# Optimization experiments

Measured on AMD Instinct MI355X. Metric: run time of the kernel, lower is better.

Reference implementation:

```python
import jax, jax.numpy as jnp
import numpy as np

D_MODEL = 768
D_STATE = 16
D_CONV = 4
D_INNER = 2 * D_MODEL          # expand=2
DT_RANK = (D_MODEL + 15) // 16 # ceil(d_model/16), official Mamba default
N_LAYERS = 4
N_VOCAB = 2048
LN_EPS = 1e-5


def _silu(x):
    return x * jax.nn.sigmoid(x)


def _layer_norm(x, g, b):
    mu = jnp.mean(x, axis=-1, keepdims=True)
    var = jnp.mean(jnp.square(x - mu), axis=-1, keepdims=True)
    return (x - mu) * jax.lax.rsqrt(var + LN_EPS) * g + b


def _mamba_block(x, W_in, conv_w, conv_b, W_x, W_dt, b_dt, A_log, D_skip, W_out):
    # x: [B, L, D_MODEL]
    Bsz, L, _ = x.shape
    xz = x @ W_in                              # [B, L, 2*D_INNER]
    xc, z = jnp.split(xz, 2, axis=-1)
    # causal depthwise conv over time
    xt = xc.transpose(0, 2, 1)                 # [B, D_INNER, L]
    kern = conv_w[:, None, :]                  # [D_INNER, 1, D_CONV]
    xt = jax.lax.conv_general_dilated(
        xt, kern, window_strides=(1,), padding=[(D_CONV - 1, 0)],
        dimension_numbers=('NCH', 'OIH', 'NCH'), feature_group_count=D_INNER)
    u = _silu(xt.transpose(0, 2, 1) + conv_b)  # [B, L, D_INNER]
    # input-dependent SSM params
    dbl = u @ W_x                              # [B, L, DT_RANK + 2*D_STATE]
    dt, Bm, Cm = jnp.split(dbl, [DT_RANK, DT_RANK + D_STATE], axis=-1)
    delta = jax.nn.softplus(dt @ W_dt + b_dt)  # [B, L, D_INNER]
    A = -jnp.exp(A_log)                        # [D_INNER, D_STATE], negative

    def step(h, inp):
        d_t, B_t, C_t, u_t = inp               # [B,Di],[B,N],[B,N],[B,Di]
        dA = jnp.exp(d_t[..., None] * A)       # [B, D_INNER, D_STATE]
        dBu = (d_t * u_t)[..., None] * B_t[:, None, :]
        h = dA * h + dBu
        y = jnp.einsum('bdn,bn->bd', h, C_t)
        return h, y

    h0 = jnp.zeros((Bsz, D_INNER, D_STATE), x.dtype)
    _, ys = jax.lax.scan(step, h0, (delta.transpose(1, 0, 2),
                                    Bm.transpose(1, 0, 2),
                                    Cm.transpose(1, 0, 2),
                                    u.transpose(1, 0, 2)))
    y = ys.transpose(1, 0, 2) + u * D_skip     # skip connection D*u
    y = y * _silu(z)                           # gating
    return y @ W_out                           # [B, L, D_MODEL]


def setup_inputs() -> dict:
    key = jax.random.key(0)
    ks = jax.random.split(key, 12)
    B, L = 2, 2048
    s = 0.02
    tokens = jax.random.randint(ks[0], (B, L), 0, N_VOCAB)
    emb = jax.random.normal(ks[1], (N_VOCAB + 1, D_MODEL), jnp.float32) * s
    emb = emb.at[N_VOCAB].set(0.0)  # padding_idx row
    in_proj_w = jax.random.normal(ks[2], (N_LAYERS, D_MODEL, 2 * D_INNER), jnp.float32) * s
    conv_w = jax.random.normal(ks[3], (N_LAYERS, D_INNER, D_CONV), jnp.float32) * s
    conv_b = jnp.zeros((N_LAYERS, D_INNER), jnp.float32)
    x_proj_w = jax.random.normal(ks[4], (N_LAYERS, D_INNER, DT_RANK + 2 * D_STATE), jnp.float32) * s
    dt_proj_w = jax.random.normal(ks[5], (N_LAYERS, DT_RANK, D_INNER), jnp.float32) * s
    # dt bias so softplus(bias) lands in [1e-3, 0.1] (standard Mamba dt init)
    dt = jnp.exp(jax.random.uniform(ks[6], (N_LAYERS, D_INNER)) * (np.log(0.1) - np.log(1e-3)) + np.log(1e-3))
    dt_proj_b = dt + jnp.log(-jnp.expm1(-dt))  # inverse softplus
    A_log = jnp.log(jnp.tile(jnp.arange(1, D_STATE + 1, dtype=jnp.float32), (N_LAYERS, D_INNER, 1)))
    skip_D = jnp.ones((N_LAYERS, D_INNER), jnp.float32)
    out_proj_w = jax.random.normal(ks[7], (N_LAYERS, D_INNER, D_MODEL), jnp.float32) * s
    ln_g = jnp.ones((N_LAYERS, D_MODEL), jnp.float32)
    ln_b = jnp.zeros((N_LAYERS, D_MODEL), jnp.float32)
    head_w = jax.random.normal(ks[8], (D_MODEL, N_VOCAB), jnp.float32) * s
    head_b = jnp.zeros((N_VOCAB,), jnp.float32)
    return dict(tokens=tokens, emb=emb, in_proj_w=in_proj_w, conv_w=conv_w,
                conv_b=conv_b, x_proj_w=x_proj_w, dt_proj_w=dt_proj_w,
                dt_proj_b=dt_proj_b, A_log=A_log, skip_D=skip_D,
                out_proj_w=out_proj_w, ln_g=ln_g, ln_b=ln_b,
                head_w=head_w, head_b=head_b)


def reference(tokens, emb, in_proj_w, conv_w, conv_b, x_proj_w, dt_proj_w,
              dt_proj_b, A_log, skip_D, out_proj_w, ln_g, ln_b, head_w, head_b):
    x = emb[tokens]                            # [B, L, D_MODEL]
    for i in range(N_LAYERS):                  # post-norm residual (prenorm=False)
        z = _mamba_block(x, in_proj_w[i], conv_w[i], conv_b[i], x_proj_w[i],
                         dt_proj_w[i], dt_proj_b[i], A_log[i], skip_D[i],
                         out_proj_w[i])
        x = x + z                              # dropout=0 (identity)
        x = _layer_norm(x, ln_g[i], ln_b[i])
    return x @ head_w + head_b                 # [B, L, N_VOCAB]
```

## Files before the change

kernel.cpp:

```cpp
#include <hip/hip_runtime.h>
#include <hip/hip_bf16.h>
#include <math.h>

#define BSZ 2
#define SEQ 2048
#define DM 768
#define DI 1536
#define DS 16
#define DTR 48
#define NL 4
#define NV 2048
#define LNEPS 1e-5f
#define MROWS (BSZ * SEQ)
#define CCH 32
#define TCH 64
#define KSPLIT 12

typedef __hip_bfloat16 bf16;
typedef unsigned short u16t;
typedef __attribute__((ext_vector_type(8))) short short8;
typedef __attribute__((ext_vector_type(4))) float f32x4;

__device__ __forceinline__ bool probe_bf16(const void* p) {
    const u16t* q = (const u16t*)p;
    return q[0] == 0x3F80 && q[1] == 0x3F80;
}
__device__ __forceinline__ float ldany(const void* p, size_t i, bool bf) {
    if (bf) {
        unsigned u = (unsigned)(((const u16t*)p)[i]) << 16;
        return __uint_as_float(u);
    }
    return ((const float*)p)[i];
}
__device__ __forceinline__ float ldb(const bf16* p, size_t i) { return __bfloat162float(p[i]); }
__device__ __forceinline__ void stb(bf16* p, size_t i, float v) { p[i] = __float2bfloat16(v); }
__device__ __forceinline__ u16t f2bbits(float f) {
    unsigned x = __float_as_uint(f);
    return (u16t)((x + 0x7fffu + ((x >> 16) & 1u)) >> 16);
}
__device__ __forceinline__ u16t ld_bfbits(const void* p, size_t i, bool bf) {
    if (bf) return ((const u16t*)p)[i];
    return f2bbits(((const float*)p)[i]);
}
__device__ __forceinline__ float softplus_fast(float x) {
    if (x > 20.f) return x;
    return 0.69314718056f * __log2f(1.f + __expf(x));
}
__device__ __forceinline__ float siluf(float x) { return x / (1.f + __expf(-x)); }

__global__ __launch_bounds__(256) void embed_kernel(const int* __restrict__ tokens,
                                                    const void* __restrict__ emb,
                                                    bf16* __restrict__ X,
                                                    const void* __restrict__ probe) {
    bool bf = probe_bf16(probe);
    int idx = blockIdx.x * 256 + threadIdx.x;
    if (idx >= MROWS * DM) return;
    int c = idx % DM;
    int bl = idx / DM;
    stb(X, idx, ldany(emb, (size_t)tokens[bl] * DM + c, bf));
}

__global__ __launch_bounds__(256) void transpose_w(const void* __restrict__ W, size_t woff,
                                                   bf16* __restrict__ WT, int K, int N,
                                                   const void* __restrict__ probe) {
    bool bf = probe_bf16(probe);
    __shared__ u16t T[64][65];
    const int n0 = blockIdx.x * 64, k0 = blockIdx.y * 64;
    const int tid = threadIdx.x;
#pragma unroll
    for (int it = 0; it < 16; ++it) {
        int j = tid + 256 * it;
        int r = j >> 6, c = j & 63;
        T[r][c] = ld_bfbits(W, woff + (size_t)(k0 + r) * N + n0 + c, bf);
    }
    __syncthreads();
#pragma unroll
    for (int it = 0; it < 2; ++it) {
        int j = tid + 256 * it;
        int c = j >> 3, r8 = (j & 7) * 8;
        u16t tmp[8];
#pragma unroll
        for (int e = 0; e < 8; ++e) tmp[e] = T[r8 + e][c];
        *reinterpret_cast<uint4*>(WT + (size_t)(n0 + c) * K + k0 + r8) =
            *reinterpret_cast<const uint4*>(tmp);
    }
}

template <int MODE>
__global__ __launch_bounds__(256) void gemm_bt(const bf16* __restrict__ A, int lda,
                                               const bf16* __restrict__ BT,
                                               const void* __restrict__ bias, size_t bioff,
                                               bf16* __restrict__ Cb, void* __restrict__ Cout,
                                               int N, int K,
                                               const void* __restrict__ probe) {
    __shared__ u16t Alds[128 * 40];
    __shared__ u16t Blds[128 * 40];
    const int tid = threadIdx.x;
    const int lane = tid & 63, w = tid >> 6;
    const int wr = w >> 1, wc = w & 1;
    const int l15 = lane & 15, l4 = lane >> 4;
    const int row0 = blockIdx.y * 128, col0 = blockIdx.x * 128;
    f32x4 acc[4][4];
#pragma unroll
    for (int i = 0; i < 4; ++i)
#pragma unroll
        for (int j = 0; j < 4; ++j) acc[i][j] = (f32x4){0.f, 0.f, 0.f, 0.f};

    for (int k0 = 0; k0 < K; k0 += 32) {
#pragma unroll
        for (int j = 0; j < 2; ++j) {
            int i = tid + 256 * j;
            int r = i >> 2, c8 = (i & 3) * 8;
            uint4 va = *reinterpret_cast<const uint4*>(A + (size_t)(row0 + r) * lda + k0 + c8);
            *reinterpret_cast<uint4*>(&Alds[r * 40 + c8]) = va;
            uint4 vb = *reinterpret_cast<const uint4*>(BT + (size_t)(col0 + r) * K + k0 + c8);
            *reinterpret_cast<uint4*>(&Blds[r * 40 + c8]) = vb;
        }
        __syncthreads();
        short8 af[4], bfr[4];
#pragma unroll
        for (int fi = 0; fi < 4; ++fi)
            af[fi] = *reinterpret_cast<const short8*>(&Alds[(wr * 64 + fi * 16 + l15) * 40 + l4 * 8]);
#pragma unroll
        for (int fj = 0; fj < 4; ++fj)
            bfr[fj] = *reinterpret_cast<const short8*>(&Blds[(wc * 64 + fj * 16 + l15) * 40 + l4 * 8]);
#pragma unroll
        for (int fi = 0; fi < 4; ++fi)
#pragma unroll
            for (int fj = 0; fj < 4; ++fj)
                acc[fi][fj] = __builtin_amdgcn_mfma_f32_16x16x32_bf16(af[fi], bfr[fj],
                                                                      acc[fi][fj], 0, 0, 0);
        __syncthreads();
    }
    bool bf = probe_bf16(probe);
#pragma unroll
    for (int fi = 0; fi < 4; ++fi) {
        int row = row0 + wr * 64 + fi * 16 + l4 * 4;
#pragma unroll
        for (int fj = 0; fj < 4; ++fj) {
            int col = col0 + wc * 64 + fj * 16 + l15;
#pragma unroll
            for (int r = 0; r < 4; ++r) {
                float v = acc[fi][fj][r];
                size_t off = (size_t)(row + r) * N + col;
                if (MODE == 2) {
                    float o = v + ldany(bias, bioff + col, bf);
                    if (bf) stb((bf16*)Cout, off, o);
                    else ((float*)Cout)[off] = o;
                } else {
                    stb(Cb, off, v);
                }
            }
        }
    }
}

__global__ __launch_bounds__(256) void xproj_mfma(const bf16* __restrict__ A,
                                                  const void* __restrict__ B, size_t boff,
                                                  float* __restrict__ XPART,
                                                  const void* __restrict__ probe) {
    bool bf = probe_bf16(probe);
    __shared__ u16t Alds[128 * 40];
    __shared__ u16t Blds[80 * 40];
    const int tid = threadIdx.x;
    const int lane = tid & 63, w = tid >> 6;
    const int l15 = lane & 15, l4 = lane >> 4;
    const int z = blockIdx.x, row0 = blockIdx.y * 128;
    f32x4 acc[2][5];
#pragma unroll
    for (int i = 0; i < 2; ++i)
#pragma unroll
        for (int j = 0; j < 5; ++j) acc[i][j] = (f32x4){0.f, 0.f, 0.f, 0.f};

    for (int ks = 0; ks < 4; ++ks) {
        int kbase = z * 128 + ks * 32;
#pragma unroll
        for (int j = 0; j < 2; ++j) {
            int i = tid + 256 * j;
            int r = i >> 2, c8 = (i & 3) * 8;
            uint4 v = *reinterpret_cast<const uint4*>(A + (size_t)(row0 + r) * DI + kbase + c8);
            *reinterpret_cast<uint4*>(&Alds[r * 40 + c8]) = v;
        }
        for (int i = tid; i < 320; i += 256) {
            int kk = i / 10, c8 = (i % 10) * 8;
            u16t tmp[8];
            if (bf) {
                uint4 v = *reinterpret_cast<const uint4*>((const u16t*)B + boff +
                                                          (size_t)(kbase + kk) * 80 + c8);
                const u16t* s = (const u16t*)&v;
#pragma unroll
                for (int e = 0; e < 8; ++e) tmp[e] = s[e];
            } else {
                const float* Bf = (const float*)B + boff + (size_t)(kbase + kk) * 80 + c8;
#pragma unroll
                for (int e = 0; e < 8; ++e) tmp[e] = f2bbits(Bf[e]);
            }
#pragma unroll
            for (int e = 0; e < 8; ++e) Blds[(c8 + e) * 40 + kk] = tmp[e];
        }
        __syncthreads();
        short8 af[2], bfr[5];
#pragma unroll
        for (int fi = 0; fi < 2; ++fi)
            af[fi] = *reinterpret_cast<const short8*>(&Alds[(w * 32 + fi * 16 + l15) * 40 + l4 * 8]);
#pragma unroll
        for (int fj = 0; fj < 5; ++fj)
            bfr[fj] = *reinterpret_cast<const short8*>(&Blds[(fj * 16 + l15) * 40 + l4 * 8]);
#pragma unroll
        for (int fi = 0; fi < 2; ++fi)
#pragma unroll
            for (int fj = 0; fj < 5; ++fj)
                acc[fi][fj] = __builtin_amdgcn_mfma_f32_16x16x32_bf16(af[fi], bfr[fj],
                                                                      acc[fi][fj], 0, 0, 0);
        __syncthreads();
    }
#pragma unroll
    for (int fi = 0; fi < 2; ++fi) {
        int row = row0 + w * 32 + fi * 16 + l4 * 4;
#pragma unroll
        for (int fj = 0; fj < 5; ++fj) {
            int col = fj * 16 + l15;
#pragma unroll
            for (int r = 0; r < 4; ++r)
                XPART[((size_t)z * MROWS + row + r) * 80 + col] = acc[fi][fj][r];
        }
    }
}

__global__ __launch_bounds__(256) void xreduce_kernel(const float* __restrict__ XPART,
                                                      bf16* __restrict__ DBL) {
    int idx = blockIdx.x * 256 + threadIdx.x;
    float s = 0.f;
#pragma unroll
    for (int z = 0; z < KSPLIT; ++z) s += XPART[(size_t)z * MROWS * 80 + idx];
    stb(DBL, idx, s);
}

__global__ __launch_bounds__(256) void dtproj_valu(const bf16* __restrict__ DBL,
                                                   const void* __restrict__ Wdt, size_t woff,
                                                   const void* __restrict__ bias, size_t bioff,
                                                   bf16* __restrict__ DELTA,
                                                   const void* __restrict__ probe) {
    bool bf = probe_bf16(probe);
    __shared__ float Wlds[48 * 132];
    __shared__ float Dlds[64 * 49];
    const int tid = threadIdx.x;
    const int tx = tid & 15, ty = tid >> 4;
    const int col0 = blockIdx.x * 128, rows0 = blockIdx.y * 64;
#pragma unroll
    for (int it = 0; it < 24; ++it) {
        int j = tid + 256 * it;
        int k = j >> 7, c = j & 127;
        Wlds[k * 132 + c] = ldany(Wdt, woff + (size_t)k * DI + col0 + c, bf);
    }
#pragma unroll
    for (int it = 0; it < 12; ++it) {
        int j = tid + 256 * it;
        int r = j / 48, k = j % 48;
        Dlds[r * 49 + k] = ldb(DBL, (size_t)(rows0 + r) * 80 + k);
    }
    __syncthreads();
    float acc[4][8] = {};
#pragma unroll 4
    for (int k = 0; k < 48; ++k) {
        float4 w0 = *reinterpret_cast<const float4*>(&Wlds[k * 132 + tx * 8]);
        float4 w1 = *reinterpret_cast<const float4*>(&Wlds[k * 132 + tx * 8 + 4]);
        float wv[8] = {w0.x, w0.y, w0.z, w0.w, w1.x, w1.y, w1.z, w1.w};
#pragma unroll
        for (int r = 0; r < 4; ++r) {
            float d = Dlds[(ty * 4 + r) * 49 + k];
#pragma unroll
            for (int e = 0; e < 8; ++e) acc[r][e] += d * wv[e];
        }
    }
    float bj[8];
#pragma unroll
    for (int e = 0; e < 8; ++e) bj[e] = ldany(bias, bioff + col0 + tx * 8 + e, bf);
#pragma unroll
    for (int r = 0; r < 4; ++r) {
        u16t tmp[8];
#pragma unroll
        for (int e = 0; e < 8; ++e) tmp[e] = f2bbits(softplus_fast(acc[r][e] + bj[e]));
        *reinterpret_cast<uint4*>(DELTA + (size_t)(rows0 + ty * 4 + r) * DI + col0 + tx * 8) =
            *reinterpret_cast<const uint4*>(tmp);
    }
}

__global__ __launch_bounds__(256) void conv_silu_kernel(const bf16* __restrict__ XZ,
                                                        const void* __restrict__ cw, size_t cwoff,
                                                        const void* __restrict__ cb, size_t cboff,
                                                        bf16* __restrict__ U,
                                                        const void* __restrict__ probe) {
    bool bf = probe_bf16(probe);
    int idx = blockIdx.x * 256 + threadIdx.x;
    if (idx >= MROWS * DI) return;
    int d = idx % DI;
    int bl = idx / DI;
    int l = bl % SEQ;
    int b = bl / SEQ;
    float s = ldany(cb, cboff + d, bf);
#pragma unroll
    for (int k = 0; k < 4; ++k) {
        int lt = l - 3 + k;
        if (lt >= 0)
            s += ldany(cw, cwoff + d * 4 + k, bf) * ldb(XZ, ((size_t)(b * SEQ + lt)) * (2 * DI) + d);
    }
    stb(U, idx, siluf(s));
}

__global__ __launch_bounds__(256) void scan_phase1(const bf16* __restrict__ DELTA,
                                                   const bf16* __restrict__ U,
                                                   const bf16* __restrict__ DBL,
                                                   const void* __restrict__ A_log, size_t aoff,
                                                   float* __restrict__ P, float* __restrict__ Q,
                                                   const void* __restrict__ probe) {
    bool bf = probe_bf16(probe);
    int blk = blockIdx.x;
    int dt = blk % (DI / 256);
    int t2 = blk / (DI / 256);
    int c = t2 % CCH;
    int b = t2 / CCH;
    int d = dt * 256 + threadIdx.x;
    float An[16], h[16], q[16];
#pragma unroll
    for (int n = 0; n < 16; ++n) {
        An[n] = -__expf(ldany(A_log, aoff + (size_t)d * DS + n, bf));
        h[n] = 0.f;
        q[n] = 1.f;
    }
    int t0 = c * TCH;
    const bf16* dp = DELTA + (size_t)(b * SEQ + t0) * DI + d;
    const bf16* up = U + (size_t)(b * SEQ + t0) * DI + d;
    const u16t* bcp = (const u16t*)DBL + (size_t)(b * SEQ + t0) * 80 + DTR;
    float del = ldb(dp, 0), u = ldb(up, 0);
    uint4 b0 = *reinterpret_cast<const uint4*>(bcp);
    uint4 b1 = *reinterpret_cast<const uint4*>(bcp + 8);
    for (int t = 0; t < TCH; ++t) {
        float delc = del, uc = u;
        uint4 c0 = b0, c1 = b1;
        if (t + 1 < TCH) {
            dp += DI; up += DI; bcp += 80;
            del = ldb(dp, 0);
            u = ldb(up, 0);
            b0 = *reinterpret_cast<const uint4*>(bcp);
            b1 = *reinterpret_cast<const uint4*>(bcp + 8);
        }
        float du = delc * uc;
        const u16t* bs0 = (const u16t*)&c0;
        const u16t* bs1 = (const u16t*)&c1;
#pragma unroll
        for (int n = 0; n < 16; ++n) {
            float Bn = __uint_as_float((unsigned)(n < 8 ? bs0[n] : bs1[n - 8]) << 16);
            float dA = __expf(delc * An[n]);
            h[n] = dA * h[n] + du * Bn;
            q[n] *= dA;
        }
    }
    size_t o = ((((size_t)b * CCH + c) * DI) + d) * 16;
#pragma unroll
    for (int n = 0; n < 16; ++n) {
        P[o + n] = h[n];
        Q[o + n] = q[n];
    }
}

__global__ __launch_bounds__(256) void scan_phase2(const float* __restrict__ P,
                                                   const float* __restrict__ Q,
                                                   float* __restrict__ H0) {
    int g = blockIdx.x * 256 + threadIdx.x;
    int n = g & 15;
    int rest = g >> 4;
    int d = rest % DI;
    int b = rest / DI;
    float S = 0.f;
    for (int c = 0; c < CCH; ++c) {
        size_t idx = ((((size_t)b * CCH + c) * DI) + d) * 16 + n;
        H0[idx] = S;
        S = Q[idx] * S + P[idx];
    }
}

__global__ __launch_bounds__(256) void scan_phase3(const bf16* __restrict__ DELTA,
                                                   bf16* __restrict__ U,
                                                   const bf16* __restrict__ DBL,
                                                   const bf16* __restrict__ XZ,
                                                   const float* __restrict__ H0,
                                                   const void* __restrict__ A_log, size_t aoff,
                                                   const void* __restrict__ Dskip, size_t doff,
                                                   const void* __restrict__ probe) {
    bool bf = probe_bf16(probe);
    int blk = blockIdx.x;
    int dt = blk % (DI / 256);
    int t2 = blk / (DI / 256);
    int c = t2 % CCH;
    int b = t2 / CCH;
    int d = dt * 256 + threadIdx.x;
    float An[16], h[16];
    size_t ho = ((((size_t)b * CCH + c) * DI) + d) * 16;
#pragma unroll
    for (int n = 0; n < 16; ++n) {
        An[n] = -__expf(ldany(A_log, aoff + (size_t)d * DS + n, bf));
        h[n] = H0[ho + n];
    }
    float Dk = ldany(Dskip, doff + d, bf);
    int t0 = c * TCH;
    const bf16* dp = DELTA + (size_t)(b * SEQ + t0) * DI + d;
    bf16* ub = U;
    const bf16* zp = XZ + (size_t)(b * SEQ + t0) * 2 * DI + DI + d;
    const u16t* bcp = (const u16t*)DBL + (size_t)(b * SEQ + t0) * 80 + DTR;
    const bf16* up = U + (size_t)(b * SEQ + t0) * DI + d;
    float del = ldb(dp, 0), u = ldb(up, 0), z = ldb(zp, 0);
    uint4 b0 = *reinterpret_cast<const uint4*>(bcp);
    uint4 b1 = *reinterpret_cast<const uint4*>(bcp + 8);
    uint4 b2 = *reinterpret_cast<const uint4*>(bcp + 16);
    uint4 b3 = *reinterpret_cast<const uint4*>(bcp + 24);
    for (int t = 0; t < TCH; ++t) {
        float delc = del, uc = u, zc = z;
        uint4 c0 = b0, c1 = b1, c2 = b2, c3 = b3;
        if (t + 1 < TCH) {
            dp += DI; up += DI; zp += 2 * DI; bcp += 80;
            del = ldb(dp, 0);
            u = ldb(up, 0);
            z = ldb(zp, 0);
            b0 = *reinterpret_cast<const uint4*>(bcp);
            b1 = *reinterpret_cast<const uint4*>(bcp + 8);
            b2 = *reinterpret_cast<const uint4*>(bcp + 16);
            b3 = *reinterpret_cast<const uint4*>(bcp + 24);
        }
        float du = delc * uc;
        const u16t* bs0 = (const u16t*)&c0;
        const u16t* bs1 = (const u16t*)&c1;
        const u16t* cs0 = (const u16t*)&c2;
        const u16t* cs1 = (const u16t*)&c3;
        float y = 0.f;
#pragma unroll
        for (int n = 0; n < 16; ++n) {
            float Bn = __uint_as_float((unsigned)(n < 8 ? bs0[n] : bs1[n - 8]) << 16);
            float Cn = __uint_as_float((unsigned)(n < 8 ? cs0[n] : cs1[n - 8]) << 16);
            float dA = __expf(delc * An[n]);
            h[n] = dA * h[n] + du * Bn;
            y += h[n] * Cn;
        }
        stb(ub, (size_t)(b * SEQ + t0 + t) * DI + d, (y + uc * Dk) * siluf(zc));
    }
}

__global__ __launch_bounds__(256) void add_ln_kernel(const bf16* __restrict__ O,
                                                     bf16* __restrict__ X,
                                                     const void* __restrict__ g, size_t goff,
                                                     const void* __restrict__ be, size_t beoff,
                                                     const void* __restrict__ probe) {
    bool bf = probe_bf16(probe);
    int row = blockIdx.x;
    __shared__ float buf[DM];
    __shared__ float wred[8];
    __shared__ float stat[2];
    float part = 0.f;
    for (int c = threadIdx.x; c < DM; c += 256) {
        float v = ldb(X, (size_t)row * DM + c) + ldb(O, (size_t)row * DM + c);
        buf[c] = v;
        part += v;
    }
    for (int o = 32; o > 0; o >>= 1) part += __shfl_down(part, o, 64);
    int wid = threadIdx.x >> 6, lane = threadIdx.x & 63;
    if (lane == 0) wred[wid] = part;
    __syncthreads();
    if (threadIdx.x == 0) {
        float s = 0.f;
        for (int i = 0; i < 4; ++i) s += wred[i];
        stat[0] = s / DM;
    }
    __syncthreads();
    float mean = stat[0];
    float p2 = 0.f;
    for (int c = threadIdx.x; c < DM; c += 256) {
        float dv = buf[c] - mean;
        p2 += dv * dv;
    }
    for (int o = 32; o > 0; o >>= 1) p2 += __shfl_down(p2, o, 64);
    if (lane == 0) wred[4 + wid] = p2;
    __syncthreads();
    if (threadIdx.x == 0) {
        float s = 0.f;
        for (int i = 0; i < 4; ++i) s += wred[4 + i];
        stat[1] = rsqrtf(s / DM + LNEPS);
    }
    __syncthreads();
    float rs = stat[1];
    for (int c = threadIdx.x; c < DM; c += 256) {
        stb(X, (size_t)row * DM + c,
            (buf[c] - mean) * rs * ldany(g, goff + c, bf) + ldany(be, beoff + c, bf));
    }
}

extern "C" void kernel_launch(void* const* d_in, const int* in_sizes, int n_in,
                              void* d_out, int out_size, void* d_ws, size_t ws_size,
                              hipStream_t stream) {
    const int* tokens = (const int*)d_in[0];
    const void* emb = d_in[1];
    const void* in_proj_w = d_in[2];
    const void* conv_w = d_in[3];
    const void* conv_b = d_in[4];
    const void* x_proj_w = d_in[5];
    const void* dt_proj_w = d_in[6];
    const void* dt_proj_b = d_in[7];
    const void* A_log = d_in[8];
    const void* skip_D = d_in[9];
    const void* out_proj_w = d_in[10];
    const void* ln_g = d_in[11];
    const void* ln_b = d_in[12];
    const void* head_w = d_in[13];
    const void* head_b = d_in[14];
    const void* probe = ln_g;

    bf16* X = (bf16*)d_ws;
    bf16* XZ = X + (size_t)MROWS * DM;
    bf16* Ub = XZ + (size_t)MROWS * 2 * DI;
    bf16* DBL = Ub + (size_t)MROWS * DI;
    bf16* DELTA = DBL + (size_t)MROWS * 80;
    bf16* O = DELTA;
    float* P = (float*)(DELTA + (size_t)MROWS * DI);
    float* Q = P + (size_t)BSZ * CCH * DI * 16;
    float* H0 = Q + (size_t)BSZ * CCH * DI * 16;
    float* XPART = P;
    bf16* WT1 = (bf16*)(H0 + (size_t)BSZ * CCH * DI * 16);
    bf16* WT2 = WT1 + (size_t)(2 * DI) * DM;

    embed_kernel<<<(MROWS * DM + 255) / 256, 256, 0, stream>>>(tokens, emb, X, probe);

    for (int i = 0; i < NL; ++i) {
        transpose_w<<<dim3(2 * DI / 64, DM / 64), 256, 0, stream>>>(
            in_proj_w, (size_t)i * DM * 2 * DI, WT1, DM, 2 * DI, probe);
        transpose_w<<<dim3(DM / 64, DI / 64), 256, 0, stream>>>(
            out_proj_w, (size_t)i * DI * DM, WT2, DI, DM, probe);
        gemm_bt<0><<<dim3(2 * DI / 128, MROWS / 128), 256, 0, stream>>>(
            X, DM, WT1, nullptr, 0, XZ, nullptr, 2 * DI, DM, probe);
        conv_silu_kernel<<<(MROWS * DI + 255) / 256, 256, 0, stream>>>(
            XZ, conv_w, (size_t)i * DI * 4, conv_b, (size_t)i * DI, Ub, probe);
        xproj_mfma<<<dim3(KSPLIT, MROWS / 128), 256, 0, stream>>>(
            Ub, x_proj_w, (size_t)i * DI * 80, XPART, probe);
        xreduce_kernel<<<(MROWS * 80) / 256, 256, 0, stream>>>(XPART, DBL);
        dtproj_valu<<<dim3(DI / 128, MROWS / 64), 256, 0, stream>>>(
            DBL, dt_proj_w, (size_t)i * DTR * DI, dt_proj_b, (size_t)i * DI, DELTA, probe);
        scan_phase1<<<BSZ * CCH * (DI / 256), 256, 0, stream>>>(
            DELTA, Ub, DBL, A_log, (size_t)i * DI * DS, P, Q, probe);
        scan_phase2<<<(BSZ * DI * 16) / 256, 256, 0, stream>>>(P, Q, H0);
        scan_phase3<<<BSZ * CCH * (DI / 256), 256, 0, stream>>>(
            DELTA, Ub, DBL, XZ, H0, A_log, (size_t)i * DI * DS, skip_D, (size_t)i * DI, probe);
        gemm_bt<0><<<dim3(DM / 128, MROWS / 128), 256, 0, stream>>>(
            Ub, DI, WT2, nullptr, 0, O, nullptr, DM, DI, probe);
        add_ln_kernel<<<MROWS, 256, 0, stream>>>(O, X, ln_g, (size_t)i * DM, ln_b,
                                                 (size_t)i * DM, probe);
    }
    transpose_w<<<dim3(NV / 64, DM / 64), 256, 0, stream>>>(head_w, 0, WT1, DM, NV, probe);
    gemm_bt<2><<<dim3(NV / 128, MROWS / 128), 256, 0, stream>>>(
        X, DM, WT1, head_b, 0, nullptr, d_out, NV, DM, probe);
}
```

Before: 1.245 ms.

## Split scan state across thread pairs and vectorize conv and layernorm kernels

The scan phases 1 and 3 now assign two threads per channel, each owning 8 of the 16 state entries, which doubles the thread count to raise parallelism and cuts per-thread registers. Phase 3 combines the two partial outputs with a lane shuffle. The conv+SiLU kernel processes 8 channels per thread with 128-bit loads and stores, and add+LayerNorm uses 192 threads holding 4 values each in registers instead of a shared buffer. The pair split duplicates the delta/u/z loads per thread pair in exchange for more occupancy.

New measurement: 1.352 ms. 8.6% more time.

```diff
diff --git a/kernel.cpp b/kernel.cpp
--- a/kernel.cpp
+++ b/kernel.cpp
@@ -34,6 +34,7 @@
 }
 __device__ __forceinline__ float ldb(const bf16* p, size_t i) { return __bfloat162float(p[i]); }
 __device__ __forceinline__ void stb(bf16* p, size_t i, float v) { p[i] = __float2bfloat16(v); }
+__device__ __forceinline__ float bits2f(u16t b) { return __uint_as_float((unsigned)b << 16); }
 __device__ __forceinline__ u16t f2bbits(float f) {
     unsigned x = __float_as_uint(f);
     return (u16t)((x + 0x7fffu + ((x >> 16) & 1u)) >> 16);
@@ -286,26 +287,37 @@
     }
 }
 
-__global__ __launch_bounds__(256) void conv_silu_kernel(const bf16* __restrict__ XZ,
-                                                        const void* __restrict__ cw, size_t cwoff,
-                                                        const void* __restrict__ cb, size_t cboff,
-                                                        bf16* __restrict__ U,
-                                                        const void* __restrict__ probe) {
+__global__ __launch_bounds__(256) void conv_silu_v8(const bf16* __restrict__ XZ,
+                                                    const void* __restrict__ cw, size_t cwoff,
+                                                    const void* __restrict__ cb, size_t cboff,
+                                                    bf16* __restrict__ U,
+                                                    const void* __restrict__ probe) {
     bool bf = probe_bf16(probe);
     int idx = blockIdx.x * 256 + threadIdx.x;
-    if (idx >= MROWS * DI) return;
-    int d = idx % DI;
-    int bl = idx / DI;
+    int dp = idx % (DI / 8);
+    int bl = idx / (DI / 8);
+    int d0 = dp * 8;
     int l = bl % SEQ;
     int b = bl / SEQ;
-    float s = ldany(cb, cboff + d, bf);
+    float s[8];
+#pragma unroll
+    for (int e = 0; e < 8; ++e) s[e] = ldany(cb, cboff + d0 + e, bf);
 #pragma unroll
     for (int k = 0; k < 4; ++k) {
         int lt = l - 3 + k;
-        if (lt >= 0)
-            s += ldany(cw, cwoff + d * 4 + k, bf) * ldb(XZ, ((size_t)(b * SEQ + lt)) * (2 * DI) + d);
-    }
-    stb(U, idx, siluf(s));
+        if (lt < 0) continue;
+        uint4 v = *reinterpret_cast<const uint4*>((const u16t*)XZ +
+                                                  (size_t)(b * SEQ + lt) * 2 * DI + d0);
+        const u16t* xv = (const u16t*)&v;
+#pragma unroll
+        for (int e = 0; e < 8; ++e)
+            s[e] += ldany(cw, cwoff + (size_t)(d0 + e) * 4 + k, bf) * bits2f(xv[e]);
+    }
+    u16t out[8];
+#pragma unroll
+    for (int e = 0; e < 8; ++e) out[e] = f2bbits(siluf(s[e]));
+    *reinterpret_cast<uint4*>((u16t*)U + (size_t)bl * DI + d0) =
+        *reinterpret_cast<const uint4*>(out);
 }
 
 __global__ __launch_bounds__(256) void scan_phase1(const bf16* __restrict__ DELTA,
@@ -316,52 +328,49 @@
                                                    const void* __restrict__ probe) {
     bool bf = probe_bf16(probe);
     int blk = blockIdx.x;
-    int dt = blk % (DI / 256);
-    int t2 = blk / (DI / 256);
+    int dt = blk % (2 * DI / 256);
+    int t2 = blk / (2 * DI / 256);
     int c = t2 % CCH;
     int b = t2 / CCH;
-    int d = dt * 256 + threadIdx.x;
-    float An[16], h[16], q[16];
-#pragma unroll
-    for (int n = 0; n < 16; ++n) {
-        An[n] = -__expf(ldany(A_log, aoff + (size_t)d * DS + n, bf));
+    int g = dt * 256 + threadIdx.x;
+    int d = g >> 1, s = g & 1;
+    float An[8], h[8], q[8];
+#pragma unroll
+    for (int n = 0; n < 8; ++n) {
+        An[n] = -__expf(ldany(A_log, aoff + (size_t)d * DS + s * 8 + n, bf));
         h[n] = 0.f;
         q[n] = 1.f;
     }
     int t0 = c * TCH;
-    const bf16* dp = DELTA + (size_t)(b * SEQ + t0) * DI + d;
+    const bf16* dpp = DELTA + (size_t)(b * SEQ + t0) * DI + d;
     const bf16* up = U + (size_t)(b * SEQ + t0) * DI + d;
-    const u16t* bcp = (const u16t*)DBL + (size_t)(b * SEQ + t0) * 80 + DTR;
-    float del = ldb(dp, 0), u = ldb(up, 0);
+    const u16t* bcp = (const u16t*)DBL + (size_t)(b * SEQ + t0) * 80 + DTR + s * 8;
+    float del = ldb(dpp, 0), u = ldb(up, 0);
     uint4 b0 = *reinterpret_cast<const uint4*>(bcp);
-    uint4 b1 = *reinterpret_cast<const uint4*>(bcp + 8);
     for (int t = 0; t < TCH; ++t) {
         float delc = del, uc = u;
-        uint4 c0 = b0, c1 = b1;
+        uint4 c0 = b0;
         if (t + 1 < TCH) {
-            dp += DI; up += DI; bcp += 80;
-            del = ldb(dp, 0);
+            dpp += DI; up += DI; bcp += 80;
+            del = ldb(dpp, 0);
             u = ldb(up, 0);
             b0 = *reinterpret_cast<const uint4*>(bcp);
-            b1 = *reinterpret_cast<const uint4*>(bcp + 8);
         }
         float du = delc * uc;
-        const u16t* bs0 = (const u16t*)&c0;
-        const u16t* bs1 = (const u16t*)&c1;
-#pragma unroll
-        for (int n = 0; n < 16; ++n) {
-            float Bn = __uint_as_float((unsigned)(n < 8 ? bs0[n] : bs1[n - 8]) << 16);
+        const u16t* bs = (const u16t*)&c0;
+#pragma unroll
+        for (int n = 0; n < 8; ++n) {
+            float Bn = bits2f(bs[n]);
             float dA = __expf(delc * An[n]);
             h[n] = dA * h[n] + du * Bn;
             q[n] *= dA;
         }
     }
-    size_t o = ((((size_t)b * CCH + c) * DI) + d) * 16;
-#pragma unroll
-    for (int n = 0; n < 16; ++n) {
-        P[o + n] = h[n];
-        Q[o + n] = q[n];
-    }
+    size_t o = ((((size_t)b * CCH + c) * DI) + d) * 16 + s * 8;
+    *reinterpret_cast<float4*>(&P[o]) = (float4){h[0], h[1], h[2], h[3]};
+    *reinterpret_cast<float4*>(&P[o + 4]) = (float4){h[4], h[5], h[6], h[7]};
+    *reinterpret_cast<float4*>(&Q[o]) = (float4){q[0], q[1], q[2], q[3]};
+    *reinterpret_cast<float4*>(&Q[o + 4]) = (float4){q[4], q[5], q[6], q[7]};
 }
 
 __global__ __launch_bounds__(256) void scan_phase2(const float* __restrict__ P,
@@ -390,107 +399,102 @@
                                                    const void* __restrict__ probe) {
     bool bf = probe_bf16(probe);
     int blk = blockIdx.x;
-    int dt = blk % (DI / 256);
-    int t2 = blk / (DI / 256);
+    int dt = blk % (2 * DI / 256);
+    int t2 = blk / (2 * DI / 256);
     int c = t2 % CCH;
     int b = t2 / CCH;
-    int d = dt * 256 + threadIdx.x;
-    float An[16], h[16];
-    size_t ho = ((((size_t)b * CCH + c) * DI) + d) * 16;
-#pragma unroll
-    for (int n = 0; n < 16; ++n) {
-        An[n] = -__expf(ldany(A_log, aoff + (size_t)d * DS + n, bf));
+    int g = dt * 256 + threadIdx.x;
+    int d = g >> 1, s = g & 1;
+    float An[8], h[8];
+    size_t ho = ((((size_t)b * CCH + c) * DI) + d) * 16 + s * 8;
+#pragma unroll
+    for (int n = 0; n < 8; ++n) {
+        An[n] = -__expf(ldany(A_log, aoff + (size_t)d * DS + s * 8 + n, bf));
         h[n] = H0[ho + n];
     }
     float Dk = ldany(Dskip, doff + d, bf);
     int t0 = c * TCH;
-    const bf16* dp = DELTA + (size_t)(b * SEQ + t0) * DI + d;
-    bf16* ub = U;
+    const bf16* dpp = DELTA + (size_t)(b * SEQ + t0) * DI + d;
     const bf16* zp = XZ + (size_t)(b * SEQ + t0) * 2 * DI + DI + d;
-    const u16t* bcp = (const u16t*)DBL + (size_t)(b * SEQ + t0) * 80 + DTR;
+    const u16t* bcp = (const u16t*)DBL + (size_t)(b * SEQ + t0) * 80 + DTR + s * 8;
     const bf16* up = U + (size_t)(b * SEQ + t0) * DI + d;
-    float del = ldb(dp, 0), u = ldb(up, 0), z = ldb(zp, 0);
+    float del = ldb(dpp, 0), u = ldb(up, 0), z = ldb(zp, 0);
     uint4 b0 = *reinterpret_cast<const uint4*>(bcp);
-    uint4 b1 = *reinterpret_cast<const uint4*>(bcp + 8);
-    uint4 b2 = *reinterpret_cast<const uint4*>(bcp + 16);
-    uint4 b3 = *reinterpret_cast<const uint4*>(bcp + 24);
+    uint4 b1 = *reinterpret_cast<const uint4*>(bcp + 16);
     for (int t = 0; t < TCH; ++t) {
         float delc = del, uc = u, zc = z;
-        uint4 c0 = b0, c1 = b1, c2 = b2, c3 = b3;
+        uint4 c0 = b0, c1 = b1;
         if (t + 1 < TCH) {
-            dp += DI; up += DI; zp += 2 * DI; bcp += 80;
-            del = ldb(dp, 0);
+            dpp += DI; up += DI; zp += 2 * DI; bcp += 80;
+            del = ldb(dpp, 0);
             u = ldb(up, 0);
             z = ldb(zp, 0);
             b0 = *reinterpret_cast<const uint4*>(bcp);
-            b1 = *reinterpret_cast<const uint4*>(bcp + 8);
-            b2 = *reinterpret_cast<const uint4*>(bcp + 16);
-            b3 = *reinterpret_cast<const uint4*>(bcp + 24);
+            b1 = *reinterpret_cast<const uint4*>(bcp + 16);
         }
         float du = delc * uc;
-        const u16t* bs0 = (const u16t*)&c0;
-        const u16t* bs1 = (const u16t*)&c1;
-        const u16t* cs0 = (const u16t*)&c2;
-        const u16t* cs1 = (const u16t*)&c3;
+        const u16t* bs = (const u16t*)&c0;
+        const u16t* cs = (const u16t*)&c1;
         float y = 0.f;
 #pragma unroll
-        for (int n = 0; n < 16; ++n) {
-            float Bn = __uint_as_float((unsigned)(n < 8 ? bs0[n] : bs1[n - 8]) << 16);
-            float Cn = __uint_as_float((unsigned)(n < 8 ? cs0[n] : cs1[n - 8]) << 16);
+        for (int n = 0; n < 8; ++n) {
+            float Bn = bits2f(bs[n]);
+            float Cn = bits2f(cs[n]);
             float dA = __expf(delc * An[n]);
             h[n] = dA * h[n] + du * Bn;
             y += h[n] * Cn;
         }
-        stb(ub, (size_t)(b * SEQ + t0 + t) * DI + d, (y + uc * Dk) * siluf(zc));
-    }
-}
-
-__global__ __launch_bounds__(256) void add_ln_kernel(const bf16* __restrict__ O,
-                                                     bf16* __restrict__ X,
-                                                     const void* __restrict__ g, size_t goff,
-                                                     const void* __restrict__ be, size_t beoff,
-                                                     const void* __restrict__ probe) {
+        y += __shfl_xor(y, 1);
+        if (s == 0)
+            stb(U, (size_t)(b * SEQ + t0 + t) * DI + d, (y + uc * Dk) * siluf(zc));
+    }
+}
+
+__global__ __launch_bounds__(192) void add_ln_v4(const bf16* __restrict__ O,
+                                                 bf16* __restrict__ X,
+                                                 const void* __restrict__ g, size_t goff,
+                                                 const void* __restrict__ be, size_t beoff,
+                                                 const void* __restrict__ probe) {
     bool bf = probe_bf16(probe);
     int row = blockIdx.x;
-    __shared__ float buf[DM];
-    __shared__ float wred[8];
-    __shared__ float stat[2];
+    int t = threadIdx.x;
+    int c0 = t * 4;
+    __shared__ float wred[6];
+    uint2 xv = *reinterpret_cast<const uint2*>((const u16t*)X + (size_t)row * DM + c0);
+    uint2 ov = *reinterpret_cast<const uint2*>((const u16t*)O + (size_t)row * DM + c0);
+    const u16t* xs = (const u16t*)&xv;
+    const u16t* os = (const u16t*)&ov;
+    float v[4];
     float part = 0.f;
-    for (int c = threadIdx.x; c < DM; c += 256) {
-        float v = ldb(X, (size_t)row * DM + c) + ldb(O, (size_t)row * DM + c);
-        buf[c] = v;
-        part += v;
-    }
+#pragma unroll
+    for (int e = 0; e < 4; ++e) {
+        v[e] = bits2f(xs[e]) + bits2f(os[e]);
+        part += v[e];
+    }
+#pragma unroll
     for (int o = 32; o > 0; o >>= 1) part += __shfl_down(part, o, 64);
-    int wid = threadIdx.x >> 6, lane = threadIdx.x & 63;
+    int wid = t >> 6, lane = t & 63;
     if (lane == 0) wred[wid] = part;
     __syncthreads();
-    if (threadIdx.x == 0) {
-        float s = 0.f;
-        for (int i = 0; i < 4; ++i) s += wred[i];
-        stat[0] = s / DM;
-    }
+    float mean = (wred[0] + wred[1] + wred[2]) * (1.f / DM);
+    float p2 = 0.f;
+#pragma unroll
+    for (int e = 0; e < 4; ++e) {
+        float dv = v[e] - mean;
+        p2 += dv * dv;
+    }
+#pragma unroll
+    for (int o = 32; o > 0; o >>= 1) p2 += __shfl_down(p2, o, 64);
+    if (lane == 0) wred[3 + wid] = p2;
     __syncthreads();
-    float mean = stat[0];
-    float p2 = 0.f;
-    for (int c = threadIdx.x; c < DM; c += 256) {
-        float dv = buf[c] - mean;
-        p2 += dv * dv;
-    }
-    for (int o = 32; o > 0; o >>= 1) p2 += __shfl_down(p2, o, 64);
-    if (lane == 0) wred[4 + wid] = p2;
-    __syncthreads();
-    if (threadIdx.x == 0) {
-        float s = 0.f;
-        for (int i = 0; i < 4; ++i) s += wred[4 + i];
-        stat[1] = rsqrtf(s / DM + LNEPS);
-    }
-    __syncthreads();
-    float rs = stat[1];
-    for (int c = threadIdx.x; c < DM; c += 256) {
-        stb(X, (size_t)row * DM + c,
-            (buf[c] - mean) * rs * ldany(g, goff + c, bf) + ldany(be, beoff + c, bf));
-    }
+    float rs = rsqrtf((wred[3] + wred[4] + wred[5]) * (1.f / DM) + LNEPS);
+    u16t out[4];
+#pragma unroll
+    for (int e = 0; e < 4; ++e)
+        out[e] = f2bbits((v[e] - mean) * rs * ldany(g, goff + c0 + e, bf) +
+                         ldany(be, beoff + c0 + e, bf));
+    *reinterpret_cast<uint2*>((u16t*)X + (size_t)row * DM + c0) =
+        *reinterpret_cast<const uint2*>(out);
 }
 
 extern "C" void kernel_launch(void* const* d_in, const int* in_sizes, int n_in,
@@ -535,22 +539,22 @@
             out_proj_w, (size_t)i * DI * DM, WT2, DI, DM, probe);
         gemm_bt<0><<<dim3(2 * DI / 128, MROWS / 128), 256, 0, stream>>>(
             X, DM, WT1, nullptr, 0, XZ, nullptr, 2 * DI, DM, probe);
-        conv_silu_kernel<<<(MROWS * DI + 255) / 256, 256, 0, stream>>>(
+        conv_silu_v8<<<(MROWS * DI / 8) / 256, 256, 0, stream>>>(
             XZ, conv_w, (size_t)i * DI * 4, conv_b, (size_t)i * DI, Ub, probe);
         xproj_mfma<<<dim3(KSPLIT, MROWS / 128), 256, 0, stream>>>(
             Ub, x_proj_w, (size_t)i * DI * 80, XPART, probe);
         xreduce_kernel<<<(MROWS * 80) / 256, 256, 0, stream>>>(XPART, DBL);
         dtproj_valu<<<dim3(DI / 128, MROWS / 64), 256, 0, stream>>>(
             DBL, dt_proj_w, (size_t)i * DTR * DI, dt_proj_b, (size_t)i * DI, DELTA, probe);
-        scan_phase1<<<BSZ * CCH * (DI / 256), 256, 0, stream>>>(
+        scan_phase1<<<BSZ * CCH * (2 * DI / 256), 256, 0, stream>>>(
             DELTA, Ub, DBL, A_log, (size_t)i * DI * DS, P, Q, probe);
         scan_phase2<<<(BSZ * DI * 16) / 256, 256, 0, stream>>>(P, Q, H0);
-        scan_phase3<<<BSZ * CCH * (DI / 256), 256, 0, stream>>>(
+        scan_phase3<<<BSZ * CCH * (2 * DI / 256), 256, 0, stream>>>(
             DELTA, Ub, DBL, XZ, H0, A_log, (size_t)i * DI * DS, skip_D, (size_t)i * DI, probe);
         gemm_bt<0><<<dim3(DM / 128, MROWS / 128), 256, 0, stream>>>(
             Ub, DI, WT2, nullptr, 0, O, nullptr, DM, DI, probe);
-        add_ln_kernel<<<MROWS, 256, 0, stream>>>(O, X, ln_g, (size_t)i * DM, ln_b,
-                                                 (size_t)i * DM, probe);
+        add_ln_v4<<<MROWS, 192, 0, stream>>>(O, X, ln_g, (size_t)i * DM, ln_b,
+                                             (size_t)i * DM, probe);
     }
     transpose_w<<<dim3(NV / 64, DM / 64), 256, 0, stream>>>(head_w, 0, WT1, DM, NV, probe);
     gemm_bt<2><<<dim3(NV / 128, MROWS / 128), 256, 0, stream>>>(
```
